# Kernel tuning notes

Measured on AMD Instinct MI355X. Metric: run time of the kernel, lower is better.

## Reference

```python
import jax, jax.numpy as jnp
import numpy as np

B, S, P = 64, 32, 49
F, E, H, V = 2048, 512, 512, 32000


def setup_inputs() -> dict:
    key = jax.random.key(0)
    ks = jax.random.split(key, 20)
    sc = 0.02
    return {
        "captions": jax.random.randint(ks[0], (B, S), 0, V),
        "features": jax.random.normal(ks[1], (B, P, F), dtype=jnp.float32),
        "embed_table": jax.random.normal(ks[2], (V, E), dtype=jnp.float32) * sc,
        "W_a": jax.random.normal(ks[3], (H, F), dtype=jnp.float32) * sc,
        "b_Wa": jnp.zeros((H,), jnp.float32),
        "U_a": jax.random.normal(ks[4], (H, H), dtype=jnp.float32) * sc,
        "b_Ua": jnp.zeros((H,), jnp.float32),
        "v_a": jax.random.normal(ks[5], (1, H), dtype=jnp.float32) * sc,
        "b_va": jnp.zeros((1,), jnp.float32),
        "W_ih": jax.random.normal(ks[6], (4 * H, E + F), dtype=jnp.float32) * sc,
        "b_ih": jnp.zeros((4 * H,), jnp.float32),
        "W_hh": jax.random.normal(ks[7], (4 * H, H), dtype=jnp.float32) * sc,
        "b_hh": jnp.zeros((4 * H,), jnp.float32),
        "fc_W": jax.random.normal(ks[8], (V, H), dtype=jnp.float32) * sc,
        "fc_b": jnp.zeros((V,), jnp.float32),
        "Wh": jax.random.normal(ks[9], (H, F), dtype=jnp.float32) * sc,
        "bh": jnp.zeros((H,), jnp.float32),
        "Wc": jax.random.normal(ks[10], (H, F), dtype=jnp.float32) * sc,
        "bc": jnp.zeros((H,), jnp.float32),
    }


def reference(captions, features, embed_table, W_a, b_Wa, U_a, b_Ua, v_a, b_va,
              W_ih, b_ih, W_hh, b_hh, fc_W, fc_b, Wh, bh, Wc, bc):
    # Embedding lookup: [B, S, E]
    embed = embed_table[captions]
    # init hidden from mean annotation
    mean_feat = jnp.mean(features, axis=1)            # [B, F]
    h0 = mean_feat @ Wh.T + bh                        # [B, H]
    c0 = mean_feat @ Wc.T + bc
    # W_a(features) is time-invariant: precompute once
    att1 = jnp.einsum('bpf,hf->bph', features, W_a) + b_Wa  # [B, P, H]

    def step(carry, word_embed):
        h, c = carry
        # Bahdanau attention
        att2 = h @ U_a.T + b_Ua                                   # [B, H]
        score = jnp.tanh(att1 + att2[:, None, :]) @ v_a[0] + b_va[0]  # [B, P]
        w = jax.nn.softmax(score, axis=1)                         # [B, P]
        context = jnp.einsum('bp,bpf->bf', w, features)           # [B, F]
        # LSTMCell (PyTorch gate order: i, f, g, o)
        x = jnp.concatenate([word_embed, context], axis=1)        # [B, E+F]
        gates = x @ W_ih.T + b_ih + h @ W_hh.T + b_hh             # [B, 4H]
        i, f, g, o = jnp.split(gates, 4, axis=1)
        c_new = jax.nn.sigmoid(f) * c + jax.nn.sigmoid(i) * jnp.tanh(g)
        h_new = jax.nn.sigmoid(o) * jnp.tanh(c_new)
        # dropout is identity at inference
        logits = h_new @ fc_W.T + fc_b                            # [B, V]
        return (h_new, c_new), (logits, w)

    _, (logits, attw) = jax.lax.scan(step, (h0, c0), jnp.swapaxes(embed, 0, 1))
    outputs = jnp.swapaxes(logits, 0, 1)       # [B, S, V]
    atten_weights = jnp.swapaxes(attw, 0, 1)   # [B, S, P]
    return outputs, atten_weights
```

## Files before the change

kernel.cpp:

```cpp
#include <hip/hip_runtime.h>
#include <hip/hip_fp16.h>

typedef _Float16 f16;
typedef _Float16 f16x2 __attribute__((ext_vector_type(2)));
typedef _Float16 f16x4 __attribute__((ext_vector_type(4)));
typedef _Float16 f16x8 __attribute__((ext_vector_type(8)));
typedef float    f32x4 __attribute__((ext_vector_type(4)));


#define GLD16(g, l)                                                        \
  __builtin_amdgcn_global_load_lds(                                        \
      (const __attribute__((address_space(1))) void*)(g),                  \
      (__attribute__((address_space(3))) void*)(l), 16, 0, 0)

static __device__ __forceinline__ float fdot2f(f16x2 a, f16x2 b, float c) {
#if __has_builtin(__builtin_amdgcn_fdot2)
  return __builtin_amdgcn_fdot2(a, b, c, false);
#else
  return c + (float)a.x * (float)b.x + (float)a.y * (float)b.y;
#endif
}

__global__ __launch_bounds__(256) void k_prep(
    const float* __restrict__ feat, const float* __restrict__ W_a,
    const float* __restrict__ W_ih, const float* __restrict__ fc_W,
    const float* __restrict__ W_hh, const float* __restrict__ U_a,
    const float* __restrict__ Wh, const float* __restrict__ Wc,
    const int* __restrict__ caps, const float* __restrict__ etab,
    f16* __restrict__ feat_h, f16* __restrict__ W_a_h,
    f16* __restrict__ W_ih_h, f16* __restrict__ fc_W_h,
    f16* __restrict__ WhhP, f16* __restrict__ UaT2,
    f16* __restrict__ Whc_h, f16* __restrict__ Aemb) {
  const long c0 = 1605632;
  const long c1 = c0 + 262144;
  const long c2 = c1 + 1310720;
  const long c3 = c2 + 4096000;
  const long c4 = c3 + 262144;
  const long c5 = c4 + 65536;
  const long c6 = c5 + 262144;
  const long c7 = c6 + 262144;
  const long c8 = c7 + 262144;
  long i = (long)blockIdx.x * 256 + threadIdx.x;
  const long stride = (long)gridDim.x * 256;
  for (; i < c8; i += stride) {
    if (i >= c3 && i < c4) {
      long ii = i - c3;
      int row = (int)(ii >> 7);
      int c4i = (int)(ii & 127);
      int g = row >> 9, j = row & 511;
      float4 v = ((const float4*)W_hh)[ii];
      f16x2 p0; p0.x = (f16)v.x; p0.y = (f16)v.y;
      f16x2 p1; p1.x = (f16)v.z; p1.y = (f16)v.w;
      long k2a = 2 * (long)c4i;
      ((f16x2*)WhhP)[(k2a * 512 + j) * 4 + g] = p0;
      ((f16x2*)WhhP)[((k2a + 1) * 512 + j) * 4 + g] = p1;
      continue;
    }
    if (i >= c4 && i < c5) {
      long ii = i - c4;
      int k = (int)(ii >> 7);
      int j0 = (int)(ii & 127) * 4;
      float4 v = ((const float4*)U_a)[ii];
      f16x2 p0; p0.x = (f16)v.x; p0.y = (f16)v.y;
      f16x2 p1; p1.x = (f16)v.z; p1.y = (f16)v.w;
      ((f16x2*)UaT2)[(long)(j0 >> 1) * 512 + k] = p0;
      ((f16x2*)UaT2)[(long)((j0 >> 1) + 1) * 512 + k] = p1;
      continue;
    }
    const float4* s; f16x4* d; long j;
    if (i < c0)      { s = (const float4*)feat; d = (f16x4*)feat_h; j = i; }
    else if (i < c1) { s = (const float4*)W_a;  d = (f16x4*)W_a_h;  j = i - c0; }
    else if (i < c2) { s = (const float4*)W_ih; d = (f16x4*)W_ih_h; j = i - c1; }
    else if (i < c3) { s = (const float4*)fc_W; d = (f16x4*)fc_W_h; j = i - c2; }
    else if (i < c6) { s = (const float4*)Wh;   d = (f16x4*)Whc_h;  j = i - c5; }
    else if (i < c7) { s = (const float4*)Wc;   d = (f16x4*)(Whc_h + 1048576l); j = i - c6; }
    else {
      long jj = i - c7;
      int n = (int)(jj >> 7), e4 = (int)(jj & 127);
      int tok = caps[n];
      s = (const float4*)(etab + (long)tok * 512); d = (f16x4*)(Aemb + (long)n * 512); j = e4;
    }
    float4 v = s[j];
    f16x4 o; o.x = (f16)v.x; o.y = (f16)v.y; o.z = (f16)v.z; o.w = (f16)v.w;
    d[j] = o;
  }
}

__global__ __launch_bounds__(256) void k_mean(const f16* __restrict__ feat_h,
                                              f16* __restrict__ mean_h) {
  int b = blockIdx.x;
  int e4 = blockIdx.y * 256 + threadIdx.x;
  const f16x4* src = (const f16x4*)(feat_h + (long)b * 49 * 2048) + e4;
  float s0 = 0.f, s1 = 0.f, s2 = 0.f, s3 = 0.f;
#pragma unroll 7
  for (int p = 0; p < 49; ++p) {
    f16x4 v = src[p * 512];
    s0 += (float)v.x; s1 += (float)v.y; s2 += (float)v.z; s3 += (float)v.w;
  }
  const float inv = 1.f / 49.f;
  f16x4 o; o.x = (f16)(s0 * inv); o.y = (f16)(s1 * inv); o.z = (f16)(s2 * inv); o.w = (f16)(s3 * inv);
  ((f16x4*)(mean_h + (long)b * 2048))[e4] = o;
}

__global__ __launch_bounds__(512) void k_h0a2p(const float* __restrict__ Rh0,
                                               const float* __restrict__ bh,
                                               const float* __restrict__ bc,
                                               const f16* __restrict__ UaT2,
                                               f16* __restrict__ hA,
                                               float* __restrict__ c_state,
                                               float* __restrict__ a2pA) {
  __shared__ f16 hsl[128];
  const int b = blockIdx.x, q = blockIdx.y, tid = threadIdx.x;
  if (tid < 128) {
    int jg = q * 128 + tid;
    float hv = Rh0[(long)b * 1024 + jg] + bh[jg];
    c_state[(long)b * 512 + jg] = Rh0[(long)b * 1024 + 512 + jg] + bc[jg];
    f16 hf = (f16)hv;
    hsl[tid] = hf;
    hA[(long)b * 512 + jg] = hf;
  }
  __syncthreads();
  const unsigned* ua = (const unsigned*)UaT2 + (long)(q * 64) * 512 + tid;
  const f16x2* hv2 = (const f16x2*)hsl;
  float s0 = 0.f, s1 = 0.f;
#pragma unroll 8
  for (int j2 = 0; j2 < 64; j2 += 2) {
    s0 = fdot2f(hv2[j2], __builtin_bit_cast(f16x2, ua[(long)j2 * 512]), s0);
    s1 = fdot2f(hv2[j2 + 1], __builtin_bit_cast(f16x2, ua[(long)(j2 + 1) * 512]), s1);
  }
  a2pA[(long)b * 2048 + q * 512 + tid] = s0 + s1;
}

__global__ __launch_bounds__(256) void k_gemm(const f16* __restrict__ A, long lda,
                                              const f16* __restrict__ Bw, long ldb,
                                              float* __restrict__ Cout, long ldc,
                                              int K, int n_mtiles) {
  __shared__ f16 As[64][40];
  __shared__ f16 Bs[64][40];
  const int tid = threadIdx.x;
  const int lane = tid & 63, wave = tid >> 6;
  const int bid = blockIdx.x;
  const long m0 = (long)(bid % n_mtiles) * 64, n0 = (long)(bid / n_mtiles) * 64;
  const int lr = tid >> 2, lc = (tid & 3) * 8;
  const int wr = (wave >> 1) * 32, wc = (wave & 1) * 32;
  f32x4 acc[2][2] = {};
  const f16* Ap = A + (m0 + lr) * lda + lc;
  const f16* Bp = Bw + (n0 + lr) * ldb + lc;
  for (int k0 = 0; k0 < K; k0 += 32) {
    uint4 av = *(const uint4*)(Ap + k0);
    uint4 bv = *(const uint4*)(Bp + k0);
    __syncthreads();
    *(uint4*)&As[lr][lc] = av;
    *(uint4*)&Bs[lr][lc] = bv;
    __syncthreads();
#pragma unroll
    for (int mi = 0; mi < 2; ++mi) {
      f16x8 af = *(const f16x8*)&As[wr + mi * 16 + (lane & 15)][(lane >> 4) * 8];
#pragma unroll
      for (int ni = 0; ni < 2; ++ni) {
        f16x8 bf = *(const f16x8*)&Bs[wc + ni * 16 + (lane & 15)][(lane >> 4) * 8];
        acc[mi][ni] = __builtin_amdgcn_mfma_f32_16x16x32_f16(af, bf, acc[mi][ni], 0, 0, 0);
      }
    }
  }
#pragma unroll
  for (int mi = 0; mi < 2; ++mi)
#pragma unroll
    for (int ni = 0; ni < 2; ++ni) {
      int row_b = wr + mi * 16 + (lane >> 4) * 4;
      long gcol = n0 + wc + ni * 16 + (lane & 15);
#pragma unroll
      for (int r = 0; r < 4; ++r)
        Cout[(m0 + row_b + r) * ldc + gcol] = acc[mi][ni][r];
    }
}

__global__ __launch_bounds__(512) void k_gemm128b(const f16* __restrict__ A, long lda,
                                                  const f16* __restrict__ Bw, long ldb,
                                                  const float* __restrict__ bias1,
                                                  const float* __restrict__ bias2,
                                                  void* __restrict__ Cout, long ldc,
                                                  int K, int mode, int n_mtiles) {
  __shared__ f16 As[8192];
  __shared__ f16 Bs[8192];
  const int tid = threadIdx.x, lane = tid & 63, wave = tid >> 6;
  const int wm = wave & 3, wn = wave >> 2;
  const int bid = blockIdx.x;
  const long m0 = (long)(bid % n_mtiles) * 128, n0 = (long)(bid / n_mtiles) * 128;
  const int c0 = wave * 128 + lane, c1 = c0 + 64;
  const int r0 = c0 >> 3, s0 = (c0 & 7) ^ (r0 & 7);
  const int r1 = c1 >> 3, s1 = (c1 & 7) ^ (r1 & 7);
  const f16* gA0 = A + (m0 + r0) * lda + s0 * 8;
  const f16* gA1 = A + (m0 + r1) * lda + s1 * 8;
  const f16* gB0 = Bw + (n0 + r0) * ldb + s0 * 8;
  const f16* gB1 = Bw + (n0 + r1) * ldb + s1 * 8;
  f16* lA0 = As + (wave * 128) * 8;
  f16* lA1 = As + (wave * 128 + 64) * 8;
  f16* lB0 = Bs + (wave * 128) * 8;
  f16* lB1 = Bs + (wave * 128 + 64) * 8;
  f32x4 acc[2][4] = {};
  for (int k0 = 0; k0 < K; k0 += 64) {
    GLD16(gA0 + k0, lA0); GLD16(gA1 + k0, lA1);
    GLD16(gB0 + k0, lB0); GLD16(gB1 + k0, lB1);
    __syncthreads();
#pragma unroll
    for (int ks = 0; ks < 2; ++ks) {
      const int sp = (ks * 4 + (lane >> 4)) ^ (lane & 7);
#pragma unroll
      for (int mi = 0; mi < 2; ++mi) {
        const int rA = wm * 32 + mi * 16 + (lane & 15);
        f16x8 af = *(const f16x8*)(As + rA * 64 + sp * 8);
#pragma unroll
        for (int ni = 0; ni < 4; ++ni) {
          const int rB = wn * 64 + ni * 16 + (lane & 15);
          f16x8 bf = *(const f16x8*)(Bs + rB * 64 + sp * 8);
          acc[mi][ni] = __builtin_amdgcn_mfma_f32_16x16x32_f16(af, bf, acc[mi][ni], 0, 0, 0);
        }
      }
    }
    __syncthreads();
  }
#pragma unroll
  for (int mi = 0; mi < 2; ++mi)
#pragma unroll
    for (int ni = 0; ni < 4; ++ni) {
      int row_b = wm * 32 + mi * 16 + (lane >> 4) * 4;
      long gcol = n0 + wn * 64 + ni * 16 + (lane & 15);
      float badd = (bias1 ? bias1[gcol] : 0.f) + (bias2 ? bias2[gcol] : 0.f);
#pragma unroll
      for (int r = 0; r < 4; ++r) {
        long grow = m0 + row_b + r;
        float v = acc[mi][ni][r] + badd;
        if (mode == 0)      ((float*)Cout)[grow * ldc + gcol] = v;
        else if (mode == 1) ((f16*)Cout)[grow * ldc + gcol] = (f16)v;
        else                ((f16*)Cout)[grow * 2048 + ((gcol & 511) << 2) + (gcol >> 9)] = (f16)v;
      }
    }
}

__global__ __launch_bounds__(512) void k_fstep(
    const f16* __restrict__ WhhP, const f16* __restrict__ UaT2,
    const float* __restrict__ b_Ua, const f16* __restrict__ att1,
    const float* __restrict__ va, const f16* __restrict__ featW4,
    const float* __restrict__ gates_x, float* __restrict__ c_state,
    const f16* __restrict__ hin, f16* __restrict__ hout,
    const float* __restrict__ a2pin, float* __restrict__ a2pout,
    f16* __restrict__ Hbuf, float* __restrict__ attw_out, int t) {
  __shared__ __align__(16) f16 hh[512];
  __shared__ float att2[512];
  __shared__ float sc[64];
  __shared__ float wl[49];
  __shared__ __align__(16) float gl4[4][128][4];
  __shared__ __align__(16) f16 hsl[128];
  const int b = blockIdx.x, q = blockIdx.y, tid = threadIdx.x;
  const int lane = tid & 63, wave = tid >> 6;
  const long n = (long)b * 32 + t;

  hh[tid] = hin[(long)b * 512 + tid];
  const float* ap = a2pin + (long)b * 2048;
  att2[tid] = b_Ua[tid] + ap[tid] + ap[512 + tid] + ap[1024 + tid] + ap[1536 + tid];
  __syncthreads();

  for (int p = wave; p < 49; p += 8) {
    const f16* arow = att1 + ((long)b * 49 + p) * 512;
    float s = 0.f;
#pragma unroll
    for (int kk = 0; kk < 8; ++kk) {
      int k = lane + kk * 64;
      float x = (float)arow[k] + att2[k];
      float e = __expf(2.f * x);
      s += va[k] * (1.f - 2.f / (e + 1.f));
    }
#pragma unroll
    for (int off = 32; off; off >>= 1) s += __shfl_xor(s, off);
    if (lane == 0) sc[p] = s;
  }
  __syncthreads();

  if (wave == 0) {
    float s = (lane < 49) ? sc[lane] : -1e30f;
    float m = s;
#pragma unroll
    for (int off = 32; off; off >>= 1) m = fmaxf(m, __shfl_xor(m, off));
    float e = (lane < 49) ? __expf(s - m) : 0.f;
    float sum = e;
#pragma unroll
    for (int off = 32; off; off >>= 1) sum += __shfl_xor(sum, off);
    float wv = e / sum;
    if (lane < 49) {
      wl[lane] = wv;
      if (q == 0) attw_out[n * 49 + lane] = wv;
    }
  }
  __syncthreads();

  const int jj = tid & 127, w = tid >> 7;
  const int jg = q * 128 + jj;
  float g0 = 0.f, g1 = 0.f, g2 = 0.f, g3 = 0.f;
  {
    const uint4* W4 = (const uint4*)WhhP;
    const f16x2* hp = (const f16x2*)hh;
#pragma unroll 8
    for (int k2 = w * 64; k2 < w * 64 + 64; ++k2) {
      uint4 wv4 = W4[(long)k2 * 512 + jg];
      f16x2 hv = hp[k2];
      g0 = fdot2f(hv, __builtin_bit_cast(f16x2, wv4.x), g0);
      g1 = fdot2f(hv, __builtin_bit_cast(f16x2, wv4.y), g1);
      g2 = fdot2f(hv, __builtin_bit_cast(f16x2, wv4.z), g2);
      g3 = fdot2f(hv, __builtin_bit_cast(f16x2, wv4.w), g3);
    }
  }
  {
    const f16* fw = featW4 + (long)(b * 49) * 2048 + q * 512 + jj * 4;
    for (int p = w; p < 49; p += 4) {
      float wp = wl[p];
      uint2 u = *(const uint2*)(fw + (long)p * 2048);
      f16x2 aa = __builtin_bit_cast(f16x2, u.x);
      f16x2 bb = __builtin_bit_cast(f16x2, u.y);
      g0 += wp * (float)aa.x; g1 += wp * (float)aa.y;
      g2 += wp * (float)bb.x; g3 += wp * (float)bb.y;
    }
  }
  {
    float4 gv4; gv4.x = g0; gv4.y = g1; gv4.z = g2; gv4.w = g3;
    *(float4*)&gl4[w][jj][0] = gv4;
  }
  __syncthreads();

  if (tid < 128) {
    int jgl = q * 128 + tid;
    const float* gx = gates_x + n * 2048;
    float G0 = gx[jgl]        + gl4[0][tid][0] + gl4[1][tid][0] + gl4[2][tid][0] + gl4[3][tid][0];
    float G1 = gx[512 + jgl]  + gl4[0][tid][1] + gl4[1][tid][1] + gl4[2][tid][1] + gl4[3][tid][1];
    float G2 = gx[1024 + jgl] + gl4[0][tid][2] + gl4[1][tid][2] + gl4[2][tid][2] + gl4[3][tid][2];
    float G3 = gx[1536 + jgl] + gl4[0][tid][3] + gl4[1][tid][3] + gl4[2][tid][3] + gl4[3][tid][3];
    float c = c_state[(long)b * 512 + jgl];
    float iv = 1.f / (1.f + __expf(-G0));
    float fv = 1.f / (1.f + __expf(-G1));
    float e2 = __expf(2.f * G2); float gg = 1.f - 2.f / (e2 + 1.f);
    float ov = 1.f / (1.f + __expf(-G3));
    c = fv * c + iv * gg;
    float e3 = __expf(2.f * c); float tc = 1.f - 2.f / (e3 + 1.f);
    float hn = ov * tc;
    c_state[(long)b * 512 + jgl] = c;
    f16 hf = (f16)hn;
    hsl[tid] = hf;
    hout[(long)b * 512 + jgl] = hf;
    Hbuf[n * 512 + jgl] = hf;
  }
  __syncthreads();

  {
    const unsigned* ua = (const unsigned*)UaT2 + (long)(q * 64) * 512 + tid;
    const f16x2* hv2 = (const f16x2*)hsl;
    float s0 = 0.f, s1 = 0.f;
#pragma unroll 8
    for (int j2 = 0; j2 < 64; j2 += 2) {
      s0 = fdot2f(hv2[j2], __builtin_bit_cast(f16x2, ua[(long)j2 * 512]), s0);
      s1 = fdot2f(hv2[j2 + 1], __builtin_bit_cast(f16x2, ua[(long)(j2 + 1) * 512]), s1);
    }
    a2pout[(long)b * 2048 + q * 512 + tid] = s0 + s1;
  }
}

extern "C" void kernel_launch(void* const* d_in, const int* in_sizes, int n_in,
                              void* d_out, int out_size, void* d_ws, size_t ws_size,
                              hipStream_t stream) {
  const int*   caps = (const int*)d_in[0];
  const float* feat = (const float*)d_in[1];
  const float* etab = (const float*)d_in[2];
  const float* W_a  = (const float*)d_in[3];
  const float* b_Wa = (const float*)d_in[4];
  const float* U_a  = (const float*)d_in[5];
  const float* b_Ua = (const float*)d_in[6];
  const float* v_a  = (const float*)d_in[7];
  const float* W_ih = (const float*)d_in[9];
  const float* b_ih = (const float*)d_in[10];
  const float* W_hh = (const float*)d_in[11];
  const float* b_hh = (const float*)d_in[12];
  const float* fc_W = (const float*)d_in[13];
  const float* fc_b = (const float*)d_in[14];
  const float* Wh   = (const float*)d_in[15];
  const float* bh   = (const float*)d_in[16];
  const float* Wc   = (const float*)d_in[17];
  const float* bc   = (const float*)d_in[18];

  char* ws = (char*)d_ws;
  size_t off = 0;
  auto alloc = [&](size_t bytes) { void* p = ws + off; off += (bytes + 255) & ~(size_t)255; return p; };
  f16* feat_h  = (f16*)alloc(6553600ull * 2);
  f16* W_a_h   = (f16*)alloc(1048576ull * 2);
  f16* W_ih_h  = (f16*)alloc(5242880ull * 2);
  f16* fc_W_h  = (f16*)alloc(16384000ull * 2);
  f16* Aemb    = (f16*)alloc(1048576ull * 2);
  f16* WhhP    = (f16*)alloc(1048576ull * 2);
  f16* UaT2    = (f16*)alloc(262144ull * 2);
  f16* Whc_h   = (f16*)alloc(2097152ull * 2);
  f16* mean_h  = (f16*)alloc(131072ull * 2);
  f16* att1_h  = (f16*)alloc(1638400ull * 2);
  f16* featW4  = (f16*)alloc(6553600ull * 2);
  float* gates_x = (float*)alloc(4194304ull * 4);
  float* Rh0   = (float*)alloc(65536ull * 4);
  f16* hA      = (f16*)alloc(32768ull * 2);
  f16* hB      = (f16*)alloc(32768ull * 2);
  float* a2pA  = (float*)alloc(131072ull * 4);
  float* a2pB  = (float*)alloc(131072ull * 4);
  float* c_state = (float*)alloc(32768ull * 4);
  f16* Hbuf    = (f16*)alloc(1048576ull * 2);
  (void)ws_size; (void)in_sizes; (void)n_in; (void)out_size;

  float* out_logits = (float*)d_out;
  float* out_attw   = out_logits + 65536000ull;

  k_prep<<<4096, 256, 0, stream>>>(feat, W_a, W_ih, fc_W, W_hh, U_a, Wh, Wc, caps, etab,
                                   feat_h, W_a_h, W_ih_h, fc_W_h, WhhP, UaT2, Whc_h, Aemb);
  k_mean<<<dim3(64, 2), 256, 0, stream>>>(feat_h, mean_h);

  k_gemm<<<16, 256, 0, stream>>>(mean_h, 2048, Whc_h, 2048, Rh0, 1024, 2048, 1);
  k_h0a2p<<<dim3(64, 4), 512, 0, stream>>>(Rh0, bh, bc, UaT2, hA, c_state, a2pA);

  k_gemm128b<<<25 * 4, 512, 0, stream>>>(feat_h, 2048, W_a_h, 2048,
                                         b_Wa, nullptr, att1_h, 512, 2048, 1, 25);
  k_gemm128b<<<25 * 16, 512, 0, stream>>>(feat_h, 2048, W_ih_h + 512, 2560,
                                          nullptr, nullptr, featW4, 0, 2048, 2, 25);
  k_gemm128b<<<16 * 16, 512, 0, stream>>>(Aemb, 512, W_ih_h, 2560,
                                          b_ih, b_hh, gates_x, 2048, 512, 0, 16);

  for (int t = 0; t < 32; ++t) {
    const f16* hin = (t & 1) ? hB : hA;
    f16* hout = (t & 1) ? hA : hB;
    const float* a2i = (t & 1) ? a2pB : a2pA;
    float* a2o = (t & 1) ? a2pA : a2pB;
    k_fstep<<<dim3(64, 4), 512, 0, stream>>>(WhhP, UaT2, b_Ua, att1_h, v_a, featW4,
                                             gates_x, c_state, hin, hout, a2i, a2o,
                                             Hbuf, out_attw, t);
  }

  k_gemm128b<<<16 * 250, 512, 0, stream>>>(Hbuf, 512, fc_W_h, 512,
                                           fc_b, nullptr, out_logits, 32000, 512, 0, 16);
}
```

Measured before the change: 902.3 us.

## Reorder per-step kernel to overlap feature and W_hh loads with attention

The per-timestep LSTM kernel now prefetches the 13 feature-weight rows into registers and runs the W_hh recurrent matvec before the attention score and softmax phase, which does not depend on either. Only the context accumulation waits for the softmax weights. The gates_x load is also moved to the start and folded into wave-group 0's accumulator. This hides global-memory latency behind the attention compute and shortens the serial critical path of each step, at the cost of more registers per thread and possible lower occupancy.

```diff
diff --git a/kernel.cpp b/kernel.cpp
--- a/kernel.cpp
+++ b/kernel.cpp
@@ -255,48 +255,29 @@
   const int b = blockIdx.x, q = blockIdx.y, tid = threadIdx.x;
   const int lane = tid & 63, wave = tid >> 6;
   const long n = (long)b * 32 + t;
+  const int jj = tid & 127, w = tid >> 7, jg = q * 128 + jj;
 
   hh[tid] = hin[(long)b * 512 + tid];
   const float* ap = a2pin + (long)b * 2048;
   att2[tid] = b_Ua[tid] + ap[tid] + ap[512 + tid] + ap[1024 + tid] + ap[1536 + tid];
   __syncthreads();
 
-  for (int p = wave; p < 49; p += 8) {
-    const f16* arow = att1 + ((long)b * 49 + p) * 512;
-    float s = 0.f;
-#pragma unroll
-    for (int kk = 0; kk < 8; ++kk) {
-      int k = lane + kk * 64;
-      float x = (float)arow[k] + att2[k];
-      float e = __expf(2.f * x);
-      s += va[k] * (1.f - 2.f / (e + 1.f));
-    }
-#pragma unroll
-    for (int off = 32; off; off >>= 1) s += __shfl_xor(s, off);
-    if (lane == 0) sc[p] = s;
-  }
-  __syncthreads();
-
-  if (wave == 0) {
-    float s = (lane < 49) ? sc[lane] : -1e30f;
-    float m = s;
-#pragma unroll
-    for (int off = 32; off; off >>= 1) m = fmaxf(m, __shfl_xor(m, off));
-    float e = (lane < 49) ? __expf(s - m) : 0.f;
-    float sum = e;
-#pragma unroll
-    for (int off = 32; off; off >>= 1) sum += __shfl_xor(sum, off);
-    float wv = e / sum;
-    if (lane < 49) {
-      wl[lane] = wv;
-      if (q == 0) attw_out[n * 49 + lane] = wv;
-    }
-  }
-  __syncthreads();
-
-  const int jj = tid & 127, w = tid >> 7;
-  const int jg = q * 128 + jj;
-  float g0 = 0.f, g1 = 0.f, g2 = 0.f, g3 = 0.f;
+  float g0, g1, g2, g3;
+  if (w == 0) {
+    const float* gx = gates_x + n * 2048;
+    g0 = gx[jg]; g1 = gx[512 + jg]; g2 = gx[1024 + jg]; g3 = gx[1536 + jg];
+  } else {
+    g0 = g1 = g2 = g3 = 0.f;
+  }
+  uint2 fwv[13];
+  {
+    const f16* fw = featW4 + (long)(b * 49) * 2048 + q * 512 + jj * 4;
+#pragma unroll
+    for (int i = 0; i < 13; ++i) {
+      int p = w + 4 * i; if (p > 48) p = 48;
+      fwv[i] = *(const uint2*)(fw + (long)p * 2048);
+    }
+  }
   {
     const uint4* W4 = (const uint4*)WhhP;
     const f16x2* hp = (const f16x2*)hh;
@@ -310,13 +291,46 @@
       g3 = fdot2f(hv, __builtin_bit_cast(f16x2, wv4.w), g3);
     }
   }
-  {
-    const f16* fw = featW4 + (long)(b * 49) * 2048 + q * 512 + jj * 4;
-    for (int p = w; p < 49; p += 4) {
+  for (int p = wave; p < 49; p += 8) {
+    const f16* arow = att1 + ((long)b * 49 + p) * 512;
+    float s = 0.f;
+#pragma unroll
+    for (int kk = 0; kk < 8; ++kk) {
+      int k = lane + kk * 64;
+      float x = (float)arow[k] + att2[k];
+      float e = __expf(2.f * x);
+      s += va[k] * (1.f - 2.f / (e + 1.f));
+    }
+#pragma unroll
+    for (int off = 32; off; off >>= 1) s += __shfl_xor(s, off);
+    if (lane == 0) sc[p] = s;
+  }
+  __syncthreads();
+
+  if (wave == 0) {
+    float s = (lane < 49) ? sc[lane] : -1e30f;
+    float m = s;
+#pragma unroll
+    for (int off = 32; off; off >>= 1) m = fmaxf(m, __shfl_xor(m, off));
+    float e = (lane < 49) ? __expf(s - m) : 0.f;
+    float sum = e;
+#pragma unroll
+    for (int off = 32; off; off >>= 1) sum += __shfl_xor(sum, off);
+    float wv = e / sum;
+    if (lane < 49) {
+      wl[lane] = wv;
+      if (q == 0) attw_out[n * 49 + lane] = wv;
+    }
+  }
+  __syncthreads();
+
+#pragma unroll
+  for (int i = 0; i < 13; ++i) {
+    int p = w + 4 * i;
+    if (p < 49) {
       float wp = wl[p];
-      uint2 u = *(const uint2*)(fw + (long)p * 2048);
-      f16x2 aa = __builtin_bit_cast(f16x2, u.x);
-      f16x2 bb = __builtin_bit_cast(f16x2, u.y);
+      f16x2 aa = __builtin_bit_cast(f16x2, fwv[i].x);
+      f16x2 bb = __builtin_bit_cast(f16x2, fwv[i].y);
       g0 += wp * (float)aa.x; g1 += wp * (float)aa.y;
       g2 += wp * (float)bb.x; g3 += wp * (float)bb.y;
     }
@@ -329,11 +343,10 @@
 
   if (tid < 128) {
     int jgl = q * 128 + tid;
-    const float* gx = gates_x + n * 2048;
-    float G0 = gx[jgl]        + gl4[0][tid][0] + gl4[1][tid][0] + gl4[2][tid][0] + gl4[3][tid][0];
-    float G1 = gx[512 + jgl]  + gl4[0][tid][1] + gl4[1][tid][1] + gl4[2][tid][1] + gl4[3][tid][1];
-    float G2 = gx[1024 + jgl] + gl4[0][tid][2] + gl4[1][tid][2] + gl4[2][tid][2] + gl4[3][tid][2];
-    float G3 = gx[1536 + jgl] + gl4[0][tid][3] + gl4[1][tid][3] + gl4[2][tid][3] + gl4[3][tid][3];
+    float G0 = gl4[0][tid][0] + gl4[1][tid][0] + gl4[2][tid][0] + gl4[3][tid][0];
+    float G1 = gl4[0][tid][1] + gl4[1][tid][1] + gl4[2][tid][1] + gl4[3][tid][1];
+    float G2 = gl4[0][tid][2] + gl4[1][tid][2] + gl4[2][tid][2] + gl4[3][tid][2];
+    float G3 = gl4[0][tid][3] + gl4[1][tid][3] + gl4[2][tid][3] + gl4[3][tid][3];
     float c = c_state[(long)b * 512 + jgl];
     float iv = 1.f / (1.f + __expf(-G0));
     float fv = 1.f / (1.f + __expf(-G1));
```

Result: faster. 830.8 us, median of 2 (-7.9%).
